# Optimization experiments

Hardware: AMD Instinct MI355X
Metric: run time of the kernel (lower is better)

## Reference

```python
import jax, jax.numpy as jnp
import numpy as np

B, K, D = 32768, 64, 64
GAIN = 1.0
LOG_2PI = float(np.log(2.0 * np.pi))


def setup_inputs() -> dict:
    key = jax.random.key(0)
    k1, k2, k3, k4 = jax.random.split(key, 4)
    return {
        "x": jax.random.normal(k1, (B, D), jnp.float32),
        "means_raw": jax.random.normal(k2, (K, D), jnp.float32),
        "scale_raw": jax.random.normal(k3, (K, D, D), jnp.float32),
        "weights_raw": jax.random.normal(k4, (K,), jnp.float32),
    }


def reference(x, means_raw, scale_raw, weights_raw):
    # EqualizedLR reparametrization: w_eff = w * gain / sqrt(fan_in)
    means = means_raw * (GAIN / np.sqrt(K * D))              # [K, D]
    pre = scale_raw * (GAIN / np.sqrt(K * D * D))            # [K, D, D]
    # ExpScaleTril (diag=False): strict lower triangle + exp(diagonal)
    dvec = jnp.exp(jnp.diagonal(pre, axis1=-2, axis2=-1))    # [K, D]
    L = jnp.tril(pre, -1) + dvec[..., :, None] * jnp.eye(D, dtype=pre.dtype)  # [K, D, D]
    # mixture logits -> log weights (EqualizedLR then softmax parametrization)
    logw = jax.nn.log_softmax(weights_raw * (GAIN / np.sqrt(K)), axis=-1)    # [K]

    # Precompute L^{-1} per component (K,D small), then whiten via one big GEMM.
    eye = jnp.broadcast_to(jnp.eye(D, dtype=L.dtype), L.shape)
    Linv = jax.scipy.linalg.solve_triangular(L, eye, lower=True)             # [K, D, D]

    diff = x[:, None, :] - means[None, :, :]                 # [B, K, D]
    z = jnp.einsum('kij,bkj->bki', Linv, diff)               # whitened residuals [B, K, D]
    maha = jnp.sum(z * z, axis=-1)                           # [B, K]
    half_log_det = jnp.sum(jnp.log(dvec), axis=-1)           # [K]
    comp_lp = -0.5 * (maha + D * LOG_2PI) - half_log_det     # [B, K]

    lp = jax.scipy.special.logsumexp(comp_lp + logw, axis=-1)  # [B]
    return -jnp.mean(lp)
```

## Files before the change

### kernel.cpp

```cpp
#include <hip/hip_runtime.h>

#define LOG_2PI 1.8378770664093453f
#define LOG2E   1.4426950408889634f

typedef __attribute__((ext_vector_type(8))) short  short8;
typedef __attribute__((ext_vector_type(4))) float  float4_;
typedef __attribute__((ext_vector_type(2))) unsigned int uint2_;

__device__ __forceinline__ unsigned short f2bf(float f) {
  unsigned u = __builtin_bit_cast(unsigned, f);
  u += 0x7fffu + ((u >> 16) & 1u);
  return (unsigned short)(u >> 16);
}
__device__ __forceinline__ float hi2f(unsigned u) {
  return __builtin_bit_cast(float, u & 0xffff0000u);
}
__device__ __forceinline__ float lo2f(unsigned u) {
  return __builtin_bit_cast(float, u << 16);
}
template <int CTRL>
__device__ __forceinline__ float dpp_add(float v) {
  int t = __builtin_amdgcn_mov_dpp(__builtin_bit_cast(int, v), CTRL, 0xf, 0xf, true);
  return v + __builtin_bit_cast(float, t);
}

__global__ __launch_bounds__(256) void gmm_setup(
    const float* __restrict__ means_raw, const float* __restrict__ scale_raw,
    const float* __restrict__ weights_raw, unsigned short* __restrict__ Wb,
    float* __restrict__ cvec, float* __restrict__ beta,
    float* __restrict__ ph, float* __restrict__ out)
{
  const int k = blockIdx.x;
  const int t = threadIdx.x;
  const int lane = t & 63;
  const int wv = t >> 6;
  const int q = lane >> 4;
  const int jj = lane & 15;

  ph[k * 512 + t] = 0.0f;
  ph[k * 512 + 256 + t] = 0.0f;
  if (k == 0 && t == 0) out[0] = 0.0f;

  __shared__ float Plt[64][68];
  __shared__ float Vt[64][68];
  __shared__ __align__(16) unsigned short Vb[64][72];
  __shared__ float dg[64], rdg[64], mu_s[64], y_s[64];

  {
    const int i = t >> 2;
    const int c0 = (t & 3) * 16;
    float4_ v4[4];
    const float4_* src = (const float4_*)(scale_raw + (size_t)k * 4096 + i * 64 + c0);
    v4[0] = src[0]; v4[1] = src[1]; v4[2] = src[2]; v4[3] = src[3];
#pragma unroll
    for (int e = 0; e < 16; ++e) {
      const int c = c0 + e;
      const float val = ((const float*)v4)[e] * (1.0f / 512.0f);
      Plt[c][i] = (c < i) ? val : 0.0f;
      if (c == i) { dg[i] = val; rdg[i] = __expf(-val); }
    }
  }
  if (t < 64) mu_s[t] = means_raw[k * 64 + t] * (1.0f / 64.0f);
  __syncthreads();

  {
    const int j = wv * 16 + jj;
    float s[16];
#pragma unroll
    for (int i = 0; i < 16; ++i) s[i] = 0.0f;
#pragma unroll
    for (int m = 0; m < 64; ++m) {
      const float rm = rdg[m];
      float vcand = (m == j) ? rm : -s[m & 15] * rm;
      const float v = __shfl(vcand, (m >> 4) * 16 + jj, 64);
      if (q == (m >> 4)) {
        Vt[j][m] = v;
        Vb[j][m] = f2bf(v);
      }
      const float4_* prow = (const float4_*)&Plt[m][16 * q];
      const float4_ p0 = prow[0], p1 = prow[1], p2 = prow[2], p3 = prow[3];
      s[0]  += p0[0] * v; s[1]  += p0[1] * v; s[2]  += p0[2] * v; s[3]  += p0[3] * v;
      s[4]  += p1[0] * v; s[5]  += p1[1] * v; s[6]  += p1[2] * v; s[7]  += p1[3] * v;
      s[8]  += p2[0] * v; s[9]  += p2[1] * v; s[10] += p2[2] * v; s[11] += p2[3] * v;
      s[12] += p3[0] * v; s[13] += p3[1] * v; s[14] += p3[2] * v; s[15] += p3[3] * v;
    }
  }
  __syncthreads();

  {
    const short8 a0 = *(const short8*)&Vb[16 * wv + jj][8 * q];
    const short8 a1 = *(const short8*)&Vb[16 * wv + jj][8 * q + 32];
#pragma unroll
    for (int t4 = 0; t4 < 4; ++t4) {
      const short8 b0 = *(const short8*)&Vb[jj + 16 * t4][8 * q];
      const short8 b1 = *(const short8*)&Vb[jj + 16 * t4][8 * q + 32];
      float4_ f = {0.f, 0.f, 0.f, 0.f};
      f = __builtin_amdgcn_mfma_f32_16x16x32_bf16(a0, b0, f, 0, 0, 0);
      f = __builtin_amdgcn_mfma_f32_16x16x32_bf16(a1, b1, f, 0, 0, 0);
#pragma unroll
      for (int r = 0; r < 4; ++r) {
        const int kd = 16 * wv + 4 * q + r;
        const int n  = jj + 16 * t4;
        const int addr = k * 4096 + (((kd >> 3) & 3) * 16 + (n & 15)) * 64
                       + (kd >> 5) * 32 + (n >> 4) * 8 + (kd & 7);
        Wb[addr] = f2bf(-0.5f * LOG2E * f[r]);
      }
    }
  }
  if (wv == 0) {
    float acc = 0.0f;
    for (int j2 = 0; j2 < 64; ++j2) acc += Vt[j2][lane] * mu_s[j2];
    y_s[lane] = acc;
  }
  __syncthreads();

  if (t < 64) {
    const int i = t;
    float ci = 0.0f;
#pragma unroll
    for (int m4 = 0; m4 < 16; ++m4) {
      const float4_ a4 = *(const float4_*)&Vt[i][4 * m4];
      const float4_ b4 = *(const float4_*)&y_s[4 * m4];
      ci += a4[0] * b4[0] + a4[1] * b4[1] + a4[2] * b4[2] + a4[3] * b4[3];
    }
    cvec[k * 64 + i] = LOG2E * ci;
    float rq  = ci * mu_s[i];
    float dgv = dg[i];
    const float wr = weights_raw[i] * 0.125f;
    float mx = wr;
#pragma unroll
    for (int d = 1; d < 64; d <<= 1) mx = fmaxf(mx, __shfl_xor(mx, d, 64));
    float se = __expf(wr - mx);
#pragma unroll
    for (int d = 1; d < 64; d <<= 1) {
      se  += __shfl_xor(se, d, 64);
      rq  += __shfl_xor(rq, d, 64);
      dgv += __shfl_xor(dgv, d, 64);
    }
    if (i == 0) {
      const float wrk  = weights_raw[k] * 0.125f;
      const float logw = wrk - mx - __logf(se);
      const float bval = -0.5f * rq - 32.0f * LOG_2PI - dgv + logw;
      beta[k] = LOG2E * (bval + 90.0f);
    }
  }
}

__global__ __launch_bounds__(512) __attribute__((amdgpu_waves_per_eu(4, 4)))
void gmm_main(
    const float* __restrict__ x, const unsigned short* __restrict__ Wb,
    const float* __restrict__ cvec, const float* __restrict__ beta,
    float* __restrict__ ph)
{
  __shared__ __align__(16) unsigned short Ai[8192];
  __shared__ __align__(16) unsigned short Xc[10240];
  __shared__ float rowacc[128];

  const int t = threadIdx.x;
  const int lane = t & 63;
  const int wv = t >> 6;
  const int q = lane >> 4;
  const int lr = lane & 15;
  const int kh = blockIdx.x & 7;
  const int rt = blockIdx.x >> 3;
  const int rowBase = rt * 128;
  const int k = kh * 8 + wv;

  {
    const int rl = t >> 2;
    const int seg = t & 3;
    const int mtile = rl >> 4;
    const int mr = rl & 15;
    const float4_* src = (const float4_*)(x + (size_t)(rowBase + rl) * 64 + seg * 16);
    const float4_ v0 = src[0], v1 = src[1], v2 = src[2], v3 = src[3];
    unsigned short h[16];
#pragma unroll
    for (int e = 0; e < 4; ++e) {
      h[e]      = f2bf(v0[e]);
      h[4 + e]  = f2bf(v1[e]);
      h[8 + e]  = f2bf(v2[e]);
      h[12 + e] = f2bf(v3[e]);
    }
    const int o0 = (2 * seg) & 3, o1 = (2 * seg + 1) & 3;
    const int ks = seg >> 1;
    short8 p0, p1;
#pragma unroll
    for (int e = 0; e < 8; ++e) { p0[e] = (short)h[e]; p1[e] = (short)h[8 + e]; }
    *(short8*)&Ai[mtile * 1024 + (o0 * 16 + mr) * 16 + ks * 8] = p0;
    *(short8*)&Ai[mtile * 1024 + (o1 * 16 + mr) * 16 + ks * 8] = p1;
#pragma unroll
    for (int e = 0; e < 16; ++e)
      Xc[mtile * 1280 + (seg * 16 + e) * 20 + mr] = h[e];
    if (t < 128) rowacc[t] = 0.0f;
  }

  short8 b[2][4];
  {
    const unsigned short* wg = Wb + (size_t)k * 4096 + lane * 64;
#pragma unroll
    for (int ks = 0; ks < 2; ++ks)
#pragma unroll
      for (int t4 = 0; t4 < 4; ++t4)
        b[ks][t4] = *(const short8*)(wg + ks * 32 + t4 * 8);
  }
  float cc[4];
#pragma unroll
  for (int t4 = 0; t4 < 4; ++t4) cc[t4] = cvec[k * 64 + lr + 16 * t4];
  const float bk = beta[k];

  __syncthreads();

#pragma unroll 2
  for (int mtile = 0; mtile < 8; ++mtile) {
    const short8 a0 = *(const short8*)&Ai[mtile * 1024 + lane * 16];
    const short8 a1 = *(const short8*)&Ai[mtile * 1024 + lane * 16 + 8];
    uint2_ xq[4];
#pragma unroll
    for (int t4 = 0; t4 < 4; ++t4)
      xq[t4] = *(const uint2_*)&Xc[mtile * 1280 + (lr + 16 * t4) * 20 + 4 * q];

    float4_ f[4];
#pragma unroll
    for (int t4 = 0; t4 < 4; ++t4) {
      const float cv = cc[t4];
      float4_ acc = {cv, cv, cv, cv};
      acc = __builtin_amdgcn_mfma_f32_16x16x32_bf16(a0, b[0][t4], acc, 0, 0, 0);
      acc = __builtin_amdgcn_mfma_f32_16x16x32_bf16(a1, b[1][t4], acc, 0, 0, 0);
      f[t4] = acc;
    }

    float xr[4][4];
#pragma unroll
    for (int t4 = 0; t4 < 4; ++t4) {
      xr[t4][0] = lo2f(xq[t4][0]);
      xr[t4][1] = hi2f(xq[t4][0]);
      xr[t4][2] = lo2f(xq[t4][1]);
      xr[t4][3] = hi2f(xq[t4][1]);
    }
    float ev[4];
#pragma unroll
    for (int r = 0; r < 4; ++r) {
      float sdot = xr[0][r] * f[0][r] + xr[1][r] * f[1][r]
                 + xr[2][r] * f[2][r] + xr[3][r] * f[3][r];
      sdot = dpp_add<0x121>(sdot);
      sdot = dpp_add<0x122>(sdot);
      sdot = dpp_add<0x124>(sdot);
      sdot = dpp_add<0x128>(sdot);
      ev[r] = exp2f(sdot + bk);
    }
    if (lr == 0) {
#pragma unroll
      for (int r = 0; r < 4; ++r)
        atomicAdd(&rowacc[mtile * 16 + 4 * q + r], ev[r]);
    }
  }

  __syncthreads();
  if (t < 128) atomicAdd(&ph[rowBase + t], rowacc[t]);
}

__global__ __launch_bounds__(256) void gmm_final(const float* __restrict__ ph,
                                                 float* __restrict__ out)
{
  const int t = threadIdx.x;
  const int r0 = blockIdx.x * 512 + t;
  float v = (__logf(ph[r0]) - 90.0f) + (__logf(ph[r0 + 256]) - 90.0f);
#pragma unroll
  for (int d = 1; d < 64; d <<= 1) v += __shfl_xor(v, d, 64);
  __shared__ float s4[4];
  if ((t & 63) == 0) s4[t >> 6] = v;
  __syncthreads();
  if (t == 0)
    atomicAdd(out, -(s4[0] + s4[1] + s4[2] + s4[3]) * (1.0f / 32768.0f));
}

extern "C" void kernel_launch(void* const* d_in, const int* in_sizes, int n_in,
                              void* d_out, int out_size, void* d_ws, size_t ws_size,
                              hipStream_t stream)
{
  const float* x           = (const float*)d_in[0];
  const float* means_raw   = (const float*)d_in[1];
  const float* scale_raw   = (const float*)d_in[2];
  const float* weights_raw = (const float*)d_in[3];
  float* out = (float*)d_out;

  char* ws = (char*)d_ws;
  unsigned short* Wb = (unsigned short*)ws;
  float* cvec        = (float*)(ws + 524288);
  float* beta        = (float*)(ws + 540672);
  float* ph          = (float*)(ws + 540928);

  gmm_setup<<<64, 256, 0, stream>>>(means_raw, scale_raw, weights_raw,
                                    Wb, cvec, beta, ph, out);
  gmm_main<<<2048, 512, 0, stream>>>(x, Wb, cvec, beta, ph);
  gmm_final<<<64, 256, 0, stream>>>(ph, out);
}
```

Baseline: 109.0 us.

## Loop all components per block and fuse final log-reduction into main kernel

Each block now owns 64 rows and loops over all 64 mixture components (8 per wave), accumulating exp terms in registers instead of splitting components across 8 blocks. Row sums are completed in shared memory, so the log and mean reduction moves into the main kernel. This removes the global partial-sum buffer, its zeroing, the global atomics and the third kernel launch. In exchange the grid shrinks to 512 blocks, and each wave reloads its component weights from global memory inside the loop.

```diff
diff --git a/kernel.cpp b/kernel.cpp
--- a/kernel.cpp
+++ b/kernel.cpp
@@ -28,7 +28,7 @@
     const float* __restrict__ means_raw, const float* __restrict__ scale_raw,
     const float* __restrict__ weights_raw, unsigned short* __restrict__ Wb,
     float* __restrict__ cvec, float* __restrict__ beta,
-    float* __restrict__ ph, float* __restrict__ out)
+    float* __restrict__ out)
 {
   const int k = blockIdx.x;
   const int t = threadIdx.x;
@@ -37,8 +37,6 @@
   const int q = lane >> 4;
   const int jj = lane & 15;
 
-  ph[k * 512 + t] = 0.0f;
-  ph[k * 512 + 256 + t] = 0.0f;
   if (k == 0 && t == 0) out[0] = 0.0f;
 
   __shared__ float Plt[64][68];
@@ -150,128 +148,119 @@
 void gmm_main(
     const float* __restrict__ x, const unsigned short* __restrict__ Wb,
     const float* __restrict__ cvec, const float* __restrict__ beta,
-    float* __restrict__ ph)
+    float* __restrict__ out)
 {
-  __shared__ __align__(16) unsigned short Ai[8192];
-  __shared__ __align__(16) unsigned short Xc[10240];
-  __shared__ float rowacc[128];
+  __shared__ __align__(16) unsigned short Ai[4096];
+  __shared__ __align__(16) unsigned short Xc[5120];
+  __shared__ float rowacc[64];
 
   const int t = threadIdx.x;
   const int lane = t & 63;
   const int wv = t >> 6;
   const int q = lane >> 4;
   const int lr = lane & 15;
-  const int kh = blockIdx.x & 7;
-  const int rt = blockIdx.x >> 3;
-  const int rowBase = rt * 128;
-  const int k = kh * 8 + wv;
-
-  {
-    const int rl = t >> 2;
-    const int seg = t & 3;
+  const int rowBase = blockIdx.x * 64;
+
+  {
+    const int rl = t >> 3;
+    const int s = t & 7;
     const int mtile = rl >> 4;
     const int mr = rl & 15;
-    const float4_* src = (const float4_*)(x + (size_t)(rowBase + rl) * 64 + seg * 16);
-    const float4_ v0 = src[0], v1 = src[1], v2 = src[2], v3 = src[3];
-    unsigned short h[16];
-#pragma unroll
-    for (int e = 0; e < 4; ++e) {
-      h[e]      = f2bf(v0[e]);
-      h[4 + e]  = f2bf(v1[e]);
-      h[8 + e]  = f2bf(v2[e]);
-      h[12 + e] = f2bf(v3[e]);
-    }
-    const int o0 = (2 * seg) & 3, o1 = (2 * seg + 1) & 3;
-    const int ks = seg >> 1;
-    short8 p0, p1;
-#pragma unroll
-    for (int e = 0; e < 8; ++e) { p0[e] = (short)h[e]; p1[e] = (short)h[8 + e]; }
-    *(short8*)&Ai[mtile * 1024 + (o0 * 16 + mr) * 16 + ks * 8] = p0;
-    *(short8*)&Ai[mtile * 1024 + (o1 * 16 + mr) * 16 + ks * 8] = p1;
-#pragma unroll
-    for (int e = 0; e < 16; ++e)
-      Xc[mtile * 1280 + (seg * 16 + e) * 20 + mr] = h[e];
-    if (t < 128) rowacc[t] = 0.0f;
-  }
-
-  short8 b[2][4];
-  {
-    const unsigned short* wg = Wb + (size_t)k * 4096 + lane * 64;
-#pragma unroll
-    for (int ks = 0; ks < 2; ++ks)
+    const float4_* src = (const float4_*)(x + (size_t)(rowBase + rl) * 64 + s * 8);
+    const float4_ v0 = src[0], v1 = src[1];
+    unsigned short h[8];
+#pragma unroll
+    for (int e = 0; e < 4; ++e) { h[e] = f2bf(v0[e]); h[4 + e] = f2bf(v1[e]); }
+    short8 p;
+#pragma unroll
+    for (int e = 0; e < 8; ++e) p[e] = (short)h[e];
+    *(short8*)&Ai[mtile * 1024 + ((s & 3) * 16 + mr) * 16 + (s >> 2) * 8] = p;
+#pragma unroll
+    for (int e = 0; e < 8; ++e)
+      Xc[mtile * 1280 + (s * 8 + e) * 20 + mr] = h[e];
+    if (t < 64) rowacc[t] = 0.0f;
+  }
+  __syncthreads();
+
+  short8 a[4][2];
+#pragma unroll
+  for (int mt = 0; mt < 4; ++mt) {
+    a[mt][0] = *(const short8*)&Ai[mt * 1024 + lane * 16];
+    a[mt][1] = *(const short8*)&Ai[mt * 1024 + lane * 16 + 8];
+  }
+
+  float sacc[4][4] = {{0,0,0,0},{0,0,0,0},{0,0,0,0},{0,0,0,0}};
+
+#pragma unroll 1
+  for (int c = 0; c < 8; ++c) {
+    const int k = wv * 8 + c;
+    short8 b[2][4];
+    {
+      const unsigned short* wg = Wb + (size_t)k * 4096 + lane * 64;
+#pragma unroll
+      for (int ks = 0; ks < 2; ++ks)
+#pragma unroll
+        for (int t4 = 0; t4 < 4; ++t4)
+          b[ks][t4] = *(const short8*)(wg + ks * 32 + t4 * 8);
+    }
+    float cc[4];
+#pragma unroll
+    for (int t4 = 0; t4 < 4; ++t4) cc[t4] = cvec[k * 64 + lr + 16 * t4];
+    const float bk = beta[k];
+
+#pragma unroll 2
+    for (int mt = 0; mt < 4; ++mt) {
+      uint2_ xq[4];
 #pragma unroll
       for (int t4 = 0; t4 < 4; ++t4)
-        b[ks][t4] = *(const short8*)(wg + ks * 32 + t4 * 8);
-  }
-  float cc[4];
-#pragma unroll
-  for (int t4 = 0; t4 < 4; ++t4) cc[t4] = cvec[k * 64 + lr + 16 * t4];
-  const float bk = beta[k];
-
-  __syncthreads();
-
-#pragma unroll 2
-  for (int mtile = 0; mtile < 8; ++mtile) {
-    const short8 a0 = *(const short8*)&Ai[mtile * 1024 + lane * 16];
-    const short8 a1 = *(const short8*)&Ai[mtile * 1024 + lane * 16 + 8];
-    uint2_ xq[4];
-#pragma unroll
-    for (int t4 = 0; t4 < 4; ++t4)
-      xq[t4] = *(const uint2_*)&Xc[mtile * 1280 + (lr + 16 * t4) * 20 + 4 * q];
-
-    float4_ f[4];
-#pragma unroll
-    for (int t4 = 0; t4 < 4; ++t4) {
-      const float cv = cc[t4];
-      float4_ acc = {cv, cv, cv, cv};
-      acc = __builtin_amdgcn_mfma_f32_16x16x32_bf16(a0, b[0][t4], acc, 0, 0, 0);
-      acc = __builtin_amdgcn_mfma_f32_16x16x32_bf16(a1, b[1][t4], acc, 0, 0, 0);
-      f[t4] = acc;
-    }
-
-    float xr[4][4];
-#pragma unroll
-    for (int t4 = 0; t4 < 4; ++t4) {
-      xr[t4][0] = lo2f(xq[t4][0]);
-      xr[t4][1] = hi2f(xq[t4][0]);
-      xr[t4][2] = lo2f(xq[t4][1]);
-      xr[t4][3] = hi2f(xq[t4][1]);
-    }
-    float ev[4];
-#pragma unroll
-    for (int r = 0; r < 4; ++r) {
-      float sdot = xr[0][r] * f[0][r] + xr[1][r] * f[1][r]
-                 + xr[2][r] * f[2][r] + xr[3][r] * f[3][r];
-      sdot = dpp_add<0x121>(sdot);
-      sdot = dpp_add<0x122>(sdot);
-      sdot = dpp_add<0x124>(sdot);
-      sdot = dpp_add<0x128>(sdot);
-      ev[r] = exp2f(sdot + bk);
-    }
-    if (lr == 0) {
+        xq[t4] = *(const uint2_*)&Xc[mt * 1280 + (lr + 16 * t4) * 20 + 4 * q];
+
+      float4_ f[4];
+#pragma unroll
+      for (int t4 = 0; t4 < 4; ++t4) {
+        const float cv = cc[t4];
+        float4_ acc = {cv, cv, cv, cv};
+        acc = __builtin_amdgcn_mfma_f32_16x16x32_bf16(a[mt][0], b[0][t4], acc, 0, 0, 0);
+        acc = __builtin_amdgcn_mfma_f32_16x16x32_bf16(a[mt][1], b[1][t4], acc, 0, 0, 0);
+        f[t4] = acc;
+      }
+
+      float xr[4][4];
+#pragma unroll
+      for (int t4 = 0; t4 < 4; ++t4) {
+        xr[t4][0] = lo2f(xq[t4][0]);
+        xr[t4][1] = hi2f(xq[t4][0]);
+        xr[t4][2] = lo2f(xq[t4][1]);
+        xr[t4][3] = hi2f(xq[t4][1]);
+      }
+#pragma unroll
+      for (int r = 0; r < 4; ++r) {
+        float sdot = xr[0][r] * f[0][r] + xr[1][r] * f[1][r]
+                   + xr[2][r] * f[2][r] + xr[3][r] * f[3][r];
+        sdot = dpp_add<0x121>(sdot);
+        sdot = dpp_add<0x122>(sdot);
+        sdot = dpp_add<0x124>(sdot);
+        sdot = dpp_add<0x128>(sdot);
+        sacc[mt][r] += exp2f(sdot + bk);
+      }
+    }
+  }
+
+  if (lr == 0) {
+#pragma unroll
+    for (int mt = 0; mt < 4; ++mt)
 #pragma unroll
       for (int r = 0; r < 4; ++r)
-        atomicAdd(&rowacc[mtile * 16 + 4 * q + r], ev[r]);
-    }
-  }
-
-  __syncthreads();
-  if (t < 128) atomicAdd(&ph[rowBase + t], rowacc[t]);
-}
-
-__global__ __launch_bounds__(256) void gmm_final(const float* __restrict__ ph,
-                                                 float* __restrict__ out)
-{
-  const int t = threadIdx.x;
-  const int r0 = blockIdx.x * 512 + t;
-  float v = (__logf(ph[r0]) - 90.0f) + (__logf(ph[r0 + 256]) - 90.0f);
-#pragma unroll
-  for (int d = 1; d < 64; d <<= 1) v += __shfl_xor(v, d, 64);
-  __shared__ float s4[4];
-  if ((t & 63) == 0) s4[t >> 6] = v;
-  __syncthreads();
-  if (t == 0)
-    atomicAdd(out, -(s4[0] + s4[1] + s4[2] + s4[3]) * (1.0f / 32768.0f));
+        atomicAdd(&rowacc[mt * 16 + 4 * q + r], sacc[mt][r]);
+  }
+  __syncthreads();
+
+  if (t < 64) {
+    float v = __logf(rowacc[t]) - 90.0f;
+#pragma unroll
+    for (int d = 1; d < 64; d <<= 1) v += __shfl_xor(v, d, 64);
+    if (t == 0) atomicAdd(out, -v * (1.0f / 32768.0f));
+  }
 }
 
 extern "C" void kernel_launch(void* const* d_in, const int* in_sizes, int n_in,
@@ -288,10 +277,8 @@
   unsigned short* Wb = (unsigned short*)ws;
   float* cvec        = (float*)(ws + 524288);
   float* beta        = (float*)(ws + 540672);
-  float* ph          = (float*)(ws + 540928);
 
   gmm_setup<<<64, 256, 0, stream>>>(means_raw, scale_raw, weights_raw,
-                                    Wb, cvec, beta, ph, out);
-  gmm_main<<<2048, 512, 0, stream>>>(x, Wb, cvec, beta, ph);
-  gmm_final<<<64, 256, 0, stream>>>(ph, out);
-}
+                                    Wb, cvec, beta, out);
+  gmm_main<<<512, 512, 0, stream>>>(x, Wb, cvec, beta, out);
+}
```

Measured after the change: 142.4 us. +30.7%, slower.
